# Kernel tuning notes

Measured on AMD Instinct MI355X. Metric: run time of the kernel, lower is better.

The kernel has to match this reference:

```python
import jax, jax.numpy as jnp
import numpy as np

D = 256      # model dim
H = 8        # heads
DK = D // H  # head dim = 32
HID = 4 * D  # mlp hidden = 1024
B, S = 8, 1024
NUM_REL = 10  # rel-pos embedding vocab, padding_idx = 9


def _ln(x, g, b):
    m = jnp.mean(x, axis=-1, keepdims=True)
    v = jnp.var(x, axis=-1, keepdims=True)
    return (x - m) * jax.lax.rsqrt(v + 1e-5) * g + b


def setup_inputs() -> dict:
    key = jax.random.key(0)
    ks = jax.random.split(key, 16)
    s = 0.02
    x = jax.random.normal(ks[0], (B, S, D), jnp.float32)
    rel_pos = jax.random.randint(ks[1], (B, S, S), 0, NUM_REL, jnp.int64)
    adj = jax.random.uniform(ks[2], (B, S, S), jnp.float32)
    # attention params (Linear weights stored as [in, out])
    Wk = jax.random.normal(ks[3], (D, D), jnp.float32) * s
    Wv = jax.random.normal(ks[4], (D, D), jnp.float32) * s
    Wq = jax.random.normal(ks[5], (D, D), jnp.float32) * s
    Wo = jax.random.normal(ks[6], (D, D), jnp.float32) * s
    bk = jnp.zeros((D,)); bv = jnp.zeros((D,)); bq = jnp.zeros((D,)); bo = jnp.zeros((D,))
    # rel-pos embedding tables [10, H], padding row 9 zeroed (padding_idx=9)
    emb_f = (jax.random.normal(ks[7], (NUM_REL, H), jnp.float32) * s).at[NUM_REL - 1].set(0.0)
    emb_b = (jax.random.normal(ks[8], (NUM_REL, H), jnp.float32) * s).at[NUM_REL - 1].set(0.0)
    # GCN-MLP params
    W1 = jax.random.normal(ks[9], (D, HID), jnp.float32) * s
    Wg = jax.random.normal(ks[10], (D, HID), jnp.float32) * s
    W2 = jax.random.normal(ks[11], (HID, D), jnp.float32) * s
    b1 = jnp.zeros((HID,)); bg = jnp.zeros((HID,)); b2 = jnp.zeros((D,))
    return {
        "x": x, "rel_pos": rel_pos, "adj": adj,
        "ln1_g": jnp.ones((D,)), "ln1_b": jnp.zeros((D,)),
        "Wk": Wk, "bk": bk, "Wv": Wv, "bv": bv, "Wq": Wq, "bq": bq,
        "Wo": Wo, "bo": bo, "emb_f": emb_f, "emb_b": emb_b,
        "ln2_g": jnp.ones((D,)), "ln2_b": jnp.zeros((D,)),
        "W1": W1, "b1": b1, "Wg": Wg, "bg": bg, "W2": W2, "b2": b2,
    }


def reference(x, rel_pos, adj, ln1_g, ln1_b, Wk, bk, Wv, bv, Wq, bq, Wo, bo,
              emb_f, emb_b, ln2_g, ln2_b, W1, b1, Wg, bg, W2, b2):
    b_, s_, _ = x.shape
    # --- self-attention block (pre-LN, residual) ---
    xn = _ln(x, ln1_g, ln1_b)
    q = (xn @ Wq + bq).reshape(b_, s_, H, DK).transpose(0, 2, 1, 3)  # [B,H,S,dk]
    k = (xn @ Wk + bk).reshape(b_, s_, H, DK).transpose(0, 2, 1, 3)
    v = (xn @ Wv + bv).reshape(b_, s_, H, DK).transpose(0, 2, 1, 3)
    # multiplicative relative-position bias: [B,S,S,H] -> [B,H,S,S]
    bias = emb_f[rel_pos] + emb_b[jnp.swapaxes(rel_pos, -2, -1)]
    bias = jnp.transpose(bias, (0, 3, 1, 2))
    scores = jnp.einsum('bhqd,bhkd->bhqk', q, k) / np.sqrt(DK).astype(np.float32)
    scores = scores * (1.0 + bias)
    p = jax.nn.softmax(scores, axis=-1)
    o = jnp.einsum('bhqk,bhkd->bhqd', p, v).transpose(0, 2, 1, 3).reshape(b_, s_, D)
    x = x + (o @ Wo + bo)
    # --- GCN feed-forward block (pre-LN, residual) ---
    xn = _ln(x, ln2_g, ln2_b)
    x1 = xn @ W1 + b1                       # [B,S,HID]
    g = xn @ Wg + bg                        # [B,S,HID]
    g1, g2 = jnp.split(g, 2, axis=-1)       # each [B,S,HID/2]
    h = x1 + jnp.concatenate([
        jnp.einsum('bij,bjd->bid', adj, g1),      # adj @ g1
        jnp.einsum('bji,bjd->bid', adj, g2),      # adj.mT @ g2
    ], axis=-1)
    h = jax.nn.relu(h)
    return x + (h @ W2 + b2)
```

## Files before the change

kernel.cpp:

```cpp
#include <hip/hip_runtime.h>
#include <hip/hip_bf16.h>

#define SS 1024
#define DD 256
#define HH 8
#define DKK 32
#define HIDD 1024
#define BB 8

typedef unsigned short ushort_t;
typedef __attribute__((ext_vector_type(8))) short bf16x8;
typedef __attribute__((ext_vector_type(4))) float f32x4;
typedef __attribute__((ext_vector_type(16))) float f32x16;

__device__ __forceinline__ ushort_t f2b(float f) {
    unsigned x = __float_as_uint(f);
    unsigned r = (x + 0x7fffu + ((x >> 16) & 1u)) >> 16;
    return (ushort_t)r;
}
__device__ __forceinline__ float b2f(ushort_t u) {
    return __uint_as_float(((unsigned)u) << 16);
}
__device__ __forceinline__ void gload16(const void* g, void* l) {
    __builtin_amdgcn_global_load_lds(
        (const __attribute__((address_space(1))) unsigned int*)g,
        (__attribute__((address_space(3))) unsigned int*)l, 16, 0, 0);
}

template<bool INBF, bool EMIT>
__global__ __launch_bounds__(256) void ln_kernel(const void* __restrict__ in,
    const float* __restrict__ gamma, const float* __restrict__ beta,
    ushort_t* __restrict__ out, ushort_t* __restrict__ raw)
{
    const int row = blockIdx.x;
    const int t = threadIdx.x;
    float v;
    if (INBF) v = b2f(((const ushort_t*)in)[(long)row * DD + t]);
    else      v = ((const float*)in)[(long)row * DD + t];
    float s = v, s2 = v * v;
#pragma unroll
    for (int off = 1; off < 64; off <<= 1) {
        s += __shfl_xor(s, off);
        s2 += __shfl_xor(s2, off);
    }
    __shared__ float w1[4], w2[4];
    if ((t & 63) == 0) { w1[t >> 6] = s; w2[t >> 6] = s2; }
    __syncthreads();
    s = w1[0] + w1[1] + w1[2] + w1[3];
    s2 = w2[0] + w2[1] + w2[2] + w2[3];
    const float mean = s * (1.f / DD);
    const float var = s2 * (1.f / DD) - mean * mean;
    const float rs = rsqrtf(var + 1e-5f);
    if (EMIT) raw[(long)row * DD + t] = f2b(v);
    out[(long)row * DD + t] = f2b((v - mean) * rs * gamma[t] + beta[t]);
}

__global__ __launch_bounds__(256) void wtrans_all(
    const float* __restrict__ Wq, const float* __restrict__ Wk,
    const float* __restrict__ Wv, const float* __restrict__ Wo,
    const float* __restrict__ W1, const float* __restrict__ Wg,
    const float* __restrict__ W2,
    ushort_t* __restrict__ WqkvT, ushort_t* __restrict__ WoT,
    ushort_t* __restrict__ W1gT, ushort_t* __restrict__ W2T,
    const float* __restrict__ bq, const float* __restrict__ bk,
    const float* __restrict__ bv, const float* __restrict__ b1,
    const float* __restrict__ bg, float* __restrict__ bqkv, float* __restrict__ b1g)
{
    int t = blockIdx.x;
    const int tid = threadIdx.x;
    if (blockIdx.x == 0) {
        for (int i = tid; i < 768; i += 256)
            bqkv[i] = (i < 256) ? bq[i] : ((i < 512) ? bk[i - 256] : bv[i - 512]);
        for (int i = tid; i < 2048; i += 256)
            b1g[i] = (i < 1024) ? b1[i] : bg[i - 1024];
    }
    const float* src; ushort_t* dst; int R, C;
    if (t < 64)        { src = Wq; dst = WqkvT;              R = DD;   C = DD; }
    else if (t < 128)  { src = Wk; dst = WqkvT + 256 * 256;  R = DD;   C = DD;   t -= 64; }
    else if (t < 192)  { src = Wv; dst = WqkvT + 512 * 256;  R = DD;   C = DD;   t -= 128; }
    else if (t < 256)  { src = Wo; dst = WoT;                R = DD;   C = DD;   t -= 192; }
    else if (t < 512)  { src = W1; dst = W1gT;               R = DD;   C = HIDD; t -= 256; }
    else if (t < 768)  { src = Wg; dst = W1gT + 1024 * 256;  R = DD;   C = HIDD; t -= 512; }
    else               { src = W2; dst = W2T;                R = HIDD; C = DD;   t -= 768; }
    const int tilesC = C >> 5;
    const int r0 = (t / tilesC) * 32, c0 = (t % tilesC) * 32;
    __shared__ float tt[32][33];
    const int i = tid >> 3, j0 = (tid & 7) << 2;
    const float4 v = *(const float4*)(src + (long)(r0 + i) * C + c0 + j0);
    tt[i][j0 + 0] = v.x; tt[i][j0 + 1] = v.y; tt[i][j0 + 2] = v.z; tt[i][j0 + 3] = v.w;
    __syncthreads();
    ushort4 o;
    o.x = f2b(tt[j0 + 0][i]); o.y = f2b(tt[j0 + 1][i]);
    o.z = f2b(tt[j0 + 2][i]); o.w = f2b(tt[j0 + 3][i]);
    *(ushort4*)(dst + (long)(c0 + i) * R + r0 + j0) = o;
}

__global__ __launch_bounds__(256) void adjconv(const float* __restrict__ adj,
    ushort_t* __restrict__ adjb, ushort_t* __restrict__ adjTb)
{
    const int c0 = blockIdx.x * 32, r0 = blockIdx.y * 32;
    const long base = (long)blockIdx.z * SS * SS;
    __shared__ float t[32][33];
    const int tid = threadIdx.x;
    const int i = tid >> 3, j0 = (tid & 7) << 2;
    const float4 v = *(const float4*)(adj + base + (long)(r0 + i) * SS + c0 + j0);
    t[i][j0 + 0] = v.x; t[i][j0 + 1] = v.y; t[i][j0 + 2] = v.z; t[i][j0 + 3] = v.w;
    ushort4 oc;
    oc.x = f2b(v.x); oc.y = f2b(v.y); oc.z = f2b(v.z); oc.w = f2b(v.w);
    *(ushort4*)(adjb + base + (long)(r0 + i) * SS + c0 + j0) = oc;
    __syncthreads();
    ushort4 ot;
    ot.x = f2b(t[j0 + 0][i]); ot.y = f2b(t[j0 + 1][i]);
    ot.z = f2b(t[j0 + 2][i]); ot.w = f2b(t[j0 + 3][i]);
    *(ushort4*)(adjTb + base + (long)(c0 + i) * SS + r0 + j0) = ot;
}

__global__ __launch_bounds__(256) void pack_kernel(const int* __restrict__ rp,
    unsigned char* __restrict__ packed)
{
    const int kt = blockIdx.x, qt = blockIdx.y, b = blockIdx.z;
    __shared__ int tA[32][33];
    __shared__ int tB[32][33];
    const int tid = threadIdx.x;
    const int i = tid >> 3;
    const int j0 = (tid & 7) << 2;
    const long base = (long)b * SS * SS;
    const int4 a4 = *(const int4*)(rp + base + (long)(qt * 32 + i) * SS + kt * 32 + j0);
    tA[i][j0 + 0] = a4.x; tA[i][j0 + 1] = a4.y; tA[i][j0 + 2] = a4.z; tA[i][j0 + 3] = a4.w;
    const int4 b4 = *(const int4*)(rp + base + (long)(kt * 32 + i) * SS + qt * 32 + j0);
    tB[i][j0 + 0] = b4.x; tB[i][j0 + 1] = b4.y; tB[i][j0 + 2] = b4.z; tB[i][j0 + 3] = b4.w;
    __syncthreads();
    uchar4 o4;
    o4.x = (unsigned char)(tA[i][j0 + 0] + 10 * tB[j0 + 0][i]);
    o4.y = (unsigned char)(tA[i][j0 + 1] + 10 * tB[j0 + 1][i]);
    o4.z = (unsigned char)(tA[i][j0 + 2] + 10 * tB[j0 + 2][i]);
    o4.w = (unsigned char)(tA[i][j0 + 3] + 10 * tB[j0 + 3][i]);
    *(uchar4*)(packed + base + (long)(qt * 32 + i) * SS + kt * 32 + j0) = o4;
}

template<int MODE, bool RELU, int BN, bool SPLITZ>
__global__ __launch_bounds__(256) void mgemm(
    const ushort_t* __restrict__ A, const ushort_t* __restrict__ BT,
    const float* __restrict__ bias, const void* __restrict__ Res,
    void* __restrict__ C, void* __restrict__ C2,
    int M, int N, int K, int lda, int ldbt, int ldc,
    long sA, long sBT, long sC, long sRes, long tbStride, int tbRows, int nsplit)
{
    int n0, m0, z;
    if (SPLITZ) {
        const int fid = blockIdx.x;
        const int glin = ((fid & 7) << 6) + (fid >> 3);
        z = glin >> 5;
        const int xy = glin & 31;
        n0 = (xy & 3) * BN;
        m0 = (xy >> 2) * 128;
    } else {
        n0 = blockIdx.x * BN; m0 = blockIdx.y * 128; z = blockIdx.z;
    }
    long coff;
    const ushort_t* Ap; const ushort_t* Bp;
    if (SPLITZ) {
        const int zb = z & 7, hf = z >> 3;
        Ap = A + (long)z * sA;
        Bp = BT + (long)zb * sBT + (long)hf * tbStride;
        coff = (long)zb * sC + (long)hf * nsplit;
    } else {
        Ap = A + (long)z * sA;
        Bp = BT + (long)z * sBT;
        coff = (long)z * sC;
    }
    const int tid = threadIdx.x, wid = tid >> 6, lane = tid & 63;
    const int wr = wid >> 1, wc = wid & 1;
    const int l4 = lane & 15, lh = lane >> 4;
    constexpr int NF = BN / 32;
    __shared__ ushort_t Asb[128 * 64];
    __shared__ ushort_t Bsb[BN * 64];
    const int srow = lane >> 3;
    const int scol = 8 * ((lane & 7) ^ srow);
    f32x4 acc[4][NF] = {};
    for (int k0 = 0; k0 < K; k0 += 64) {
#pragma unroll
        for (int i = 0; i < 4; i++) {
            const int l = wid * 4 + i;
            gload16(Ap + (long)(m0 + l * 8 + srow) * lda + k0 + scol, &Asb[l * 512]);
        }
#pragma unroll
        for (int i = 0; i < NF; i++) {
            const int l = wid * NF + i;
            gload16(Bp + (long)(n0 + l * 8 + srow) * ldbt + k0 + scol, &Bsb[l * 512]);
        }
        __syncthreads();
        bf16x8 af[2][4], bfr[2][NF];
#pragma unroll
        for (int mi = 0; mi < 4; mi++) {
            const int row = wr * 64 + mi * 16 + l4;
            const int sw = (row & 7) << 3;
            af[0][mi] = *(const bf16x8*)&Asb[row * 64 + ((lh * 8) ^ sw)];
            af[1][mi] = *(const bf16x8*)&Asb[row * 64 + ((32 + lh * 8) ^ sw)];
        }
#pragma unroll
        for (int nj = 0; nj < NF; nj++) {
            const int row = wc * (BN / 2) + nj * 16 + l4;
            const int sw = (row & 7) << 3;
            bfr[0][nj] = *(const bf16x8*)&Bsb[row * 64 + ((lh * 8) ^ sw)];
            bfr[1][nj] = *(const bf16x8*)&Bsb[row * 64 + ((32 + lh * 8) ^ sw)];
        }
        __builtin_amdgcn_s_setprio(1);
#pragma unroll
        for (int kk = 0; kk < 2; kk++)
#pragma unroll
            for (int mi = 0; mi < 4; mi++)
#pragma unroll
                for (int nj = 0; nj < NF; nj++)
                    acc[mi][nj] = __builtin_amdgcn_mfma_f32_16x16x32_bf16(
                        af[kk][mi], bfr[kk][nj], acc[mi][nj], 0, 0, 0);
        __builtin_amdgcn_s_setprio(0);
        __syncthreads();
    }
#pragma unroll
    for (int mi = 0; mi < 4; mi++) {
#pragma unroll
        for (int nj = 0; nj < NF; nj++) {
            const int n = n0 + wc * (BN / 2) + nj * 16 + l4;
            const int mb = m0 + wr * 64 + mi * 16 + lh * 4;
            const float bv = bias ? bias[n] : 0.f;
            if (MODE == 1) {
                ushort_t* Cp = (ushort_t*)C + coff;
                const ushort_t* Rp = Res ? (const ushort_t*)Res + coff : (const ushort_t*)0;
#pragma unroll
                for (int r = 0; r < 4; r++) {
                    float v = acc[mi][nj][r] + bv;
                    if (Rp) v += b2f(Rp[(long)(mb + r) * ldc + n]);
                    if (RELU) v = fmaxf(v, 0.f);
                    Cp[(long)(mb + r) * ldc + n] = f2b(v);
                }
            } else if (MODE == 4) {
                float* Cp = (float*)C;
                const ushort_t* Rp = (const ushort_t*)Res;
#pragma unroll
                for (int r = 0; r < 4; r++) {
                    float v = acc[mi][nj][r] + bv + b2f(Rp[(long)(mb + r) * ldc + n]);
                    if (RELU) v = fmaxf(v, 0.f);
                    Cp[(long)(mb + r) * ldc + n] = v;
                }
            } else {
                const int nb = n0 + wc * (BN / 2) + nj * 16;
                if (nb < nsplit) {
                    ushort_t* Cp = (ushort_t*)C;
#pragma unroll
                    for (int r = 0; r < 4; r++)
                        Cp[(long)(mb + r) * ldc + n] = f2b(acc[mi][nj][r] + bv);
                } else {
                    ushort_t* Cp = (ushort_t*)C2;
                    const int bidx = mb / tbRows;
                    const int s = mb - bidx * tbRows;
                    ushort4 o4;
                    o4.x = f2b(acc[mi][nj][0] + bv);
                    o4.y = f2b(acc[mi][nj][1] + bv);
                    o4.z = f2b(acc[mi][nj][2] + bv);
                    o4.w = f2b(acc[mi][nj][3] + bv);
                    *(ushort4*)(Cp + (long)bidx * tbStride + (long)(n - nsplit) * tbRows + s) = o4;
                }
            }
        }
    }
}

__global__ __launch_bounds__(256) void attn3(
    const ushort_t* __restrict__ qk, const ushort_t* __restrict__ vt,
    const unsigned char* __restrict__ pkd,
    const float* __restrict__ ef, const float* __restrict__ eb,
    ushort_t* __restrict__ ob)
{
    const int fid = blockIdx.x;
    const int glin = ((fid & 7) << 8) + (fid >> 3);
    const int bh = glin >> 5;
    const int qt = glin & 31;
    const int b = bh >> 3, h = bh & 7;
    const int tid = threadIdx.x;
    const int wid = tid >> 6, lane = tid & 63;
    const int l31 = lane & 31, hi = lane >> 5;
    __shared__ float tm[100];
    __shared__ float cacc[3][64][20];
    __shared__ float cl[3][64];
    if (tid < 100)
        tm[tid] = 0.25506953899092946f
                  * (1.f + ef[(tid % 10) * HH + h] + eb[(tid / 10) * HH + h]);
    __syncthreads();
    const int q0 = qt * 32;
    const ushort_t* qrow = qk + ((long)(b * SS + q0 + l31)) * 512 + h * DKK + hi * 8;
    const bf16x8 qlo = *(const bf16x8*)(qrow);
    const bf16x8 qhi = *(const bf16x8*)(qrow + 16);
    const unsigned char* prow = pkd + ((long)(b * SS + q0 + l31)) * SS;
    const ushort_t* vrow = vt + ((long)(b * DD + h * DKK + l31)) * SS + hi * 8;
    const ushort_t* krow = qk + ((long)(b * SS + l31)) * 512 + 256 + h * DKK + hi * 8;
    f32x16 acc = {};
    float lrun = 0.f;
    const int kbase = wid * 256;
#pragma unroll 2
    for (int it = 0; it < 8; it++) {
        const int kt = kbase + it * 32;
        const ushort_t* kp = krow + (long)kt * 512;
        const bf16x8 klo = *(const bf16x8*)kp;
        const bf16x8 khi = *(const bf16x8*)(kp + 16);
        f32x16 sf = {};
        __builtin_amdgcn_s_setprio(1);
        sf = __builtin_amdgcn_mfma_f32_32x32x16_bf16(klo, qlo, sf, 0, 0, 0);
        sf = __builtin_amdgcn_mfma_f32_32x32x16_bf16(khi, qhi, sf, 0, 0, 0);
        __builtin_amdgcn_s_setprio(0);
        const uint4 u0 = *(const uint4*)(prow + kt);
        const uint4 u1 = *(const uint4*)(prow + kt + 16);
        const unsigned wa = hi ? u0.y : u0.x;
        const unsigned wb = hi ? u0.w : u0.z;
        const unsigned wc2 = hi ? u1.y : u1.x;
        const unsigned wd = hi ? u1.w : u1.z;
        float p[16];
#pragma unroll
        for (int rb = 0; rb < 4; rb++) {
            p[0 + rb]  = __builtin_amdgcn_exp2f(sf[0 + rb]  * tm[(wa  >> (8 * rb)) & 255u]);
            p[4 + rb]  = __builtin_amdgcn_exp2f(sf[4 + rb]  * tm[(wb  >> (8 * rb)) & 255u]);
            p[8 + rb]  = __builtin_amdgcn_exp2f(sf[8 + rb]  * tm[(wc2 >> (8 * rb)) & 255u]);
            p[12 + rb] = __builtin_amdgcn_exp2f(sf[12 + rb] * tm[(wd  >> (8 * rb)) & 255u]);
        }
        float ts = 0.f;
#pragma unroll
        for (int r = 0; r < 16; r++) ts += p[r];
        lrun += ts + __shfl_xor(ts, 32);
        unsigned cw[8];
#pragma unroll
        for (int i = 0; i < 8; i++)
            asm("v_cvt_pk_bf16_f32 %0, %1, %2" : "=v"(cw[i]) : "v"(p[2 * i]), "v"(p[2 * i + 1]));
        unsigned dw[8];
#pragma unroll
        for (int i = 0; i < 8; i++) dw[i] = (unsigned)__shfl_xor((int)cw[i], 32);
        union { unsigned u[8]; bf16x8 v[2]; } fu;
        fu.u[0] = hi ? dw[2] : cw[0]; fu.u[1] = hi ? dw[3] : cw[1];
        fu.u[2] = hi ? cw[2] : dw[0]; fu.u[3] = hi ? cw[3] : dw[1];
        fu.u[4] = hi ? dw[6] : cw[4]; fu.u[5] = hi ? dw[7] : cw[5];
        fu.u[6] = hi ? cw[6] : dw[4]; fu.u[7] = hi ? cw[7] : dw[5];
        const bf16x8 vlo = *(const bf16x8*)(vrow + kt);
        const bf16x8 vhi = *(const bf16x8*)(vrow + kt + 16);
        __builtin_amdgcn_s_setprio(1);
        acc = __builtin_amdgcn_mfma_f32_32x32x16_bf16(vlo, fu.v[0], acc, 0, 0, 0);
        acc = __builtin_amdgcn_mfma_f32_32x32x16_bf16(vhi, fu.v[1], acc, 0, 0, 0);
        __builtin_amdgcn_s_setprio(0);
    }
    if (wid != 0) {
        float* cp = &cacc[wid - 1][lane][0];
#pragma unroll
        for (int r = 0; r < 16; r++) cp[r] = acc[r];
        cl[wid - 1][lane] = lrun;
    }
    __syncthreads();
    if (wid == 0) {
#pragma unroll
        for (int w = 0; w < 3; w++) {
            const float* cp = &cacc[w][lane][0];
#pragma unroll
            for (int r = 0; r < 16; r++) acc[r] += cp[r];
            lrun += cl[w][lane];
        }
        const float invl = 1.f / lrun;
        ushort_t* orow = ob + ((long)(b * SS + q0 + l31)) * DD + h * DKK + 4 * hi;
#pragma unroll
        for (int g = 0; g < 4; g++) {
            ushort4 o4;
            o4.x = f2b(acc[4 * g + 0] * invl);
            o4.y = f2b(acc[4 * g + 1] * invl);
            o4.z = f2b(acc[4 * g + 2] * invl);
            o4.w = f2b(acc[4 * g + 3] * invl);
            *(ushort4*)(orow + 8 * g) = o4;
        }
    }
}

extern "C" void kernel_launch(void* const* d_in, const int* in_sizes, int n_in,
                              void* d_out, int out_size, void* d_ws, size_t ws_size,
                              hipStream_t stream)
{
    const float* x    = (const float*)d_in[0];
    const int*   rp   = (const int*)d_in[1];
    const float* adj  = (const float*)d_in[2];
    const float* ln1g = (const float*)d_in[3];
    const float* ln1b = (const float*)d_in[4];
    const float* Wk   = (const float*)d_in[5];
    const float* bk   = (const float*)d_in[6];
    const float* Wv   = (const float*)d_in[7];
    const float* bv   = (const float*)d_in[8];
    const float* Wq   = (const float*)d_in[9];
    const float* bq   = (const float*)d_in[10];
    const float* Wo   = (const float*)d_in[11];
    const float* bo   = (const float*)d_in[12];
    const float* embf = (const float*)d_in[13];
    const float* embb = (const float*)d_in[14];
    const float* ln2g = (const float*)d_in[15];
    const float* ln2b = (const float*)d_in[16];
    const float* W1   = (const float*)d_in[17];
    const float* b1   = (const float*)d_in[18];
    const float* Wg   = (const float*)d_in[19];
    const float* bg   = (const float*)d_in[20];
    const float* W2   = (const float*)d_in[21];
    const float* b2   = (const float*)d_in[22];
    float* out = (float*)d_out;

    char* ws = (char*)d_ws;
    const long MB = 1ll << 20;
    ushort_t* qkb = (ushort_t*)(ws + 0);
    ushort_t* vtb = (ushort_t*)(ws + 8 * MB);
    ushort_t* obb = (ushort_t*)(ws + 12 * MB);
    unsigned char* pkb = (unsigned char*)(ws + 16 * MB);
    ushort_t* xnb = (ushort_t*)(ws + 24 * MB);
    ushort_t* xb  = (ushort_t*)(ws + 28 * MB);
    ushort_t* x1hb = (ushort_t*)(ws + 0);
    ushort_t* gtb  = (ushort_t*)(ws + 16 * MB);
    ushort_t* x2b  = (ushort_t*)(ws + 32 * MB);
    ushort_t* xn2b = (ushort_t*)(ws + 36 * MB);
    ushort_t* adjb  = (ushort_t*)(ws + 40 * MB);
    ushort_t* adjTb = (ushort_t*)(ws + 56 * MB);
    ushort_t* wT    = (ushort_t*)(ws + 72 * MB);
    ushort_t* WqkvT = wT;
    ushort_t* WoT   = wT + 768 * 256;
    ushort_t* W1gT  = wT + 768 * 256 + 256 * 256;
    ushort_t* W2T   = W1gT + 2048 * 256;
    float* bqkv = (float*)(ws + 75 * MB);
    float* b1g  = bqkv + 768;

    const int rows = BB * SS;
    dim3 blk(256);

    wtrans_all<<<1024, blk, 0, stream>>>(Wq, Wk, Wv, Wo, W1, Wg, W2,
                                         WqkvT, WoT, W1gT, W2T,
                                         bq, bk, bv, b1, bg, bqkv, b1g);
    ln_kernel<false, true><<<rows, blk, 0, stream>>>(x, ln1g, ln1b, xnb, xb);
    mgemm<3, false, 64, false><<<dim3(12, 64, 1), blk, 0, stream>>>(
        xnb, WqkvT, bqkv, nullptr, qkb, vtb, rows, 768, DD, DD, DD, 512,
        0, 0, 0, 0, (long)DD * SS, SS, 512);
    pack_kernel<<<dim3(32, 32, 8), blk, 0, stream>>>(rp, pkb);
    adjconv<<<dim3(32, 32, 8), blk, 0, stream>>>(adj, adjb, adjTb);
    attn3<<<dim3(2048, 1, 1), blk, 0, stream>>>(qkb, vtb, pkb, embf, embb, obb);
    mgemm<1, false, 64, false><<<dim3(4, 64, 1), blk, 0, stream>>>(
        obb, WoT, bo, xb, x2b, nullptr, rows, DD, DD, DD, DD, DD,
        0, 0, 0, 0, 0, 1, 0);
    ln_kernel<true, false><<<rows, blk, 0, stream>>>(x2b, ln2g, ln2b, xn2b, nullptr);
    mgemm<3, false, 128, false><<<dim3(16, 64, 1), blk, 0, stream>>>(
        xn2b, W1gT, b1g, nullptr, x1hb, gtb, rows, 2048, DD, DD, DD, HIDD,
        0, 0, 0, 0, (long)HIDD * SS, SS, 1024);
    mgemm<1, true, 128, true><<<dim3(512, 1, 1), blk, 0, stream>>>(
        adjb, gtb, nullptr, x1hb, x1hb, nullptr, SS, 512, SS, SS, SS, HIDD,
        (long)SS * SS, (long)HIDD * SS, (long)SS * HIDD, 0, (long)512 * SS, SS, 512);
    mgemm<4, false, 64, false><<<dim3(4, 64, 1), blk, 0, stream>>>(
        x1hb, W2T, b2, x2b, out, nullptr, rows, DD, HIDD, HIDD, HIDD, DD,
        0, 0, 0, 0, 0, 1, 0);
}
```

Measured before the change: 337.5 us.

## Store K, V and packed rel-pos in MFMA-fragment tiled layouts for attention

The QKV GEMM epilogue now writes Q row-major, and writes K and V^T into per-(batch,head,32-key) 1KB tiles ordered to match the MFMA operand lanes. The pack kernel likewise stores packed relative-position bytes in 32x32 tiles that match the score fragment layout. The attention loop can then fetch K, V and bias indices with contiguous per-lane 16-byte loads instead of strided row gathers, which aims to improve coalescing and cut memory transactions. In exchange the K stores in the GEMM epilogue become scattered 2-byte writes.

```diff
diff --git a/kernel.cpp b/kernel.cpp
--- a/kernel.cpp
+++ b/kernel.cpp
@@ -135,14 +135,16 @@
     o4.y = (unsigned char)(tA[i][j0 + 1] + 10 * tB[j0 + 1][i]);
     o4.z = (unsigned char)(tA[i][j0 + 2] + 10 * tB[j0 + 2][i]);
     o4.w = (unsigned char)(tA[i][j0 + 3] + 10 * tB[j0 + 3][i]);
-    *(uchar4*)(packed + base + (long)(qt * 32 + i) * SS + kt * 32 + j0) = o4;
+    unsigned char* tile = packed + (((long)b * 32 + qt) * 32 + kt) * 1024;
+    const int jw = j0 >> 3, hi2 = (j0 >> 2) & 1;
+    *(uchar4*)(tile + ((hi2 * 32 + i) * 16) + jw * 4) = o4;
 }
 
 template<int MODE, bool RELU, int BN, bool SPLITZ>
 __global__ __launch_bounds__(256) void mgemm(
     const ushort_t* __restrict__ A, const ushort_t* __restrict__ BT,
     const float* __restrict__ bias, const void* __restrict__ Res,
-    void* __restrict__ C, void* __restrict__ C2,
+    void* __restrict__ C, void* __restrict__ C2, void* __restrict__ C3,
     int M, int N, int K, int lda, int ldbt, int ldc,
     long sA, long sBT, long sC, long sRes, long tbStride, int tbRows, int nsplit)
 {
@@ -242,6 +244,41 @@
                     float v = acc[mi][nj][r] + bv + b2f(Rp[(long)(mb + r) * ldc + n]);
                     if (RELU) v = fmaxf(v, 0.f);
                     Cp[(long)(mb + r) * ldc + n] = v;
+                }
+            } else if (MODE == 5) {
+                const int nb = n0 + wc * (BN / 2) + nj * 16;
+                if (nb < 256) {
+                    ushort_t* Cp = (ushort_t*)C;
+#pragma unroll
+                    for (int r = 0; r < 4; r++)
+                        Cp[(long)(mb + r) * 256 + n] = f2b(acc[mi][nj][r] + bv);
+                } else if (nb < 512) {
+                    ushort_t* Cp = (ushort_t*)C2;
+                    const int h = (n - 256) >> 5, dk = (n - 256) & 31;
+                    const int khalf = dk >> 4, hi2 = (dk >> 3) & 1, e = dk & 7;
+#pragma unroll
+                    for (int r = 0; r < 4; r++) {
+                        const int m = mb + r;
+                        const int bz = m >> 10, s = m & 1023;
+                        const long off = (((long)(bz * 8 + h) * 32 + (s >> 5)) << 10)
+                                       + khalf * 512 + (hi2 * 32 + (s & 31)) * 8 + e;
+                        Cp[off] = f2b(acc[mi][nj][r] + bv);
+                    }
+                } else {
+                    ushort_t* Cp = (ushort_t*)C3;
+                    const int d = n - 512;
+                    const int h = d >> 5, dr = d & 31;
+                    const int bz = mb >> 10, s = mb & 1023;
+                    const int kt32 = s >> 5, kc = s & 31;
+                    const int khalf = kc >> 4, hi2 = (kc >> 3) & 1, e = kc & 7;
+                    const long off = (((long)(bz * 8 + h) * 32 + kt32) << 10)
+                                   + khalf * 512 + (hi2 * 32 + dr) * 8 + e;
+                    ushort4 o4;
+                    o4.x = f2b(acc[mi][nj][0] + bv);
+                    o4.y = f2b(acc[mi][nj][1] + bv);
+                    o4.z = f2b(acc[mi][nj][2] + bv);
+                    o4.w = f2b(acc[mi][nj][3] + bv);
+                    *(ushort4*)(Cp + off) = o4;
                 }
             } else {
                 const int nb = n0 + wc * (BN / 2) + nj * 16;
@@ -267,8 +304,8 @@
 }
 
 __global__ __launch_bounds__(256) void attn3(
-    const ushort_t* __restrict__ qk, const ushort_t* __restrict__ vt,
-    const unsigned char* __restrict__ pkd,
+    const ushort_t* __restrict__ qb, const ushort_t* __restrict__ ktb,
+    const ushort_t* __restrict__ vtb, const unsigned char* __restrict__ pkt,
     const float* __restrict__ ef, const float* __restrict__ eb,
     ushort_t* __restrict__ ob)
 {
@@ -288,39 +325,34 @@
                   * (1.f + ef[(tid % 10) * HH + h] + eb[(tid / 10) * HH + h]);
     __syncthreads();
     const int q0 = qt * 32;
-    const ushort_t* qrow = qk + ((long)(b * SS + q0 + l31)) * 512 + h * DKK + hi * 8;
+    const ushort_t* qrow = qb + ((long)(b * SS + q0 + l31)) * 256 + h * DKK + hi * 8;
     const bf16x8 qlo = *(const bf16x8*)(qrow);
     const bf16x8 qhi = *(const bf16x8*)(qrow + 16);
-    const unsigned char* prow = pkd + ((long)(b * SS + q0 + l31)) * SS;
-    const ushort_t* vrow = vt + ((long)(b * DD + h * DKK + l31)) * SS + hi * 8;
-    const ushort_t* krow = qk + ((long)(b * SS + l31)) * 512 + 256 + h * DKK + hi * 8;
+    const ushort_t* kbase = ktb + (((long)(b * 8 + h) * 32) << 10);
+    const ushort_t* vbase = vtb + (((long)(b * 8 + h) * 32) << 10);
+    const unsigned char* pbase = pkt + (((long)(b * 32 + qt) * 32) << 10);
+    const int lane8 = lane * 8;
     f32x16 acc = {};
     float lrun = 0.f;
-    const int kbase = wid * 256;
 #pragma unroll 2
     for (int it = 0; it < 8; it++) {
-        const int kt = kbase + it * 32;
-        const ushort_t* kp = krow + (long)kt * 512;
-        const bf16x8 klo = *(const bf16x8*)kp;
-        const bf16x8 khi = *(const bf16x8*)(kp + 16);
+        const int kt32 = wid * 8 + it;
+        const ushort_t* ktile = kbase + (kt32 << 10);
+        const bf16x8 klo = *(const bf16x8*)(ktile + lane8);
+        const bf16x8 khi = *(const bf16x8*)(ktile + 512 + lane8);
         f32x16 sf = {};
         __builtin_amdgcn_s_setprio(1);
         sf = __builtin_amdgcn_mfma_f32_32x32x16_bf16(klo, qlo, sf, 0, 0, 0);
         sf = __builtin_amdgcn_mfma_f32_32x32x16_bf16(khi, qhi, sf, 0, 0, 0);
         __builtin_amdgcn_s_setprio(0);
-        const uint4 u0 = *(const uint4*)(prow + kt);
-        const uint4 u1 = *(const uint4*)(prow + kt + 16);
-        const unsigned wa = hi ? u0.y : u0.x;
-        const unsigned wb = hi ? u0.w : u0.z;
-        const unsigned wc2 = hi ? u1.y : u1.x;
-        const unsigned wd = hi ? u1.w : u1.z;
+        const uint4 pw = *(const uint4*)(pbase + (kt32 << 10) + lane * 16);
         float p[16];
 #pragma unroll
         for (int rb = 0; rb < 4; rb++) {
-            p[0 + rb]  = __builtin_amdgcn_exp2f(sf[0 + rb]  * tm[(wa  >> (8 * rb)) & 255u]);
-            p[4 + rb]  = __builtin_amdgcn_exp2f(sf[4 + rb]  * tm[(wb  >> (8 * rb)) & 255u]);
-            p[8 + rb]  = __builtin_amdgcn_exp2f(sf[8 + rb]  * tm[(wc2 >> (8 * rb)) & 255u]);
-            p[12 + rb] = __builtin_amdgcn_exp2f(sf[12 + rb] * tm[(wd  >> (8 * rb)) & 255u]);
+            p[0 + rb]  = __builtin_amdgcn_exp2f(sf[0 + rb]  * tm[(pw.x >> (8 * rb)) & 255u]);
+            p[4 + rb]  = __builtin_amdgcn_exp2f(sf[4 + rb]  * tm[(pw.y >> (8 * rb)) & 255u]);
+            p[8 + rb]  = __builtin_amdgcn_exp2f(sf[8 + rb]  * tm[(pw.z >> (8 * rb)) & 255u]);
+            p[12 + rb] = __builtin_amdgcn_exp2f(sf[12 + rb] * tm[(pw.w >> (8 * rb)) & 255u]);
         }
         float ts = 0.f;
 #pragma unroll
@@ -338,8 +370,9 @@
         fu.u[2] = hi ? cw[2] : dw[0]; fu.u[3] = hi ? cw[3] : dw[1];
         fu.u[4] = hi ? dw[6] : cw[4]; fu.u[5] = hi ? dw[7] : cw[5];
         fu.u[6] = hi ? cw[6] : dw[4]; fu.u[7] = hi ? cw[7] : dw[5];
-        const bf16x8 vlo = *(const bf16x8*)(vrow + kt);
-        const bf16x8 vhi = *(const bf16x8*)(vrow + kt + 16);
+        const ushort_t* vtile = vbase + (kt32 << 10);
+        const bf16x8 vlo = *(const bf16x8*)(vtile + lane8);
+        const bf16x8 vhi = *(const bf16x8*)(vtile + 512 + lane8);
         __builtin_amdgcn_s_setprio(1);
         acc = __builtin_amdgcn_mfma_f32_32x32x16_bf16(vlo, fu.v[0], acc, 0, 0, 0);
         acc = __builtin_amdgcn_mfma_f32_32x32x16_bf16(vhi, fu.v[1], acc, 0, 0, 0);
@@ -405,10 +438,11 @@
 
     char* ws = (char*)d_ws;
     const long MB = 1ll << 20;
-    ushort_t* qkb = (ushort_t*)(ws + 0);
+    ushort_t* qbb = (ushort_t*)(ws + 0);
+    ushort_t* ktb = (ushort_t*)(ws + 4 * MB);
     ushort_t* vtb = (ushort_t*)(ws + 8 * MB);
-    ushort_t* obb = (ushort_t*)(ws + 12 * MB);
-    unsigned char* pkb = (unsigned char*)(ws + 16 * MB);
+    unsigned char* pkt = (unsigned char*)(ws + 12 * MB);
+    ushort_t* obb = (ushort_t*)(ws + 20 * MB);
     ushort_t* xnb = (ushort_t*)(ws + 24 * MB);
     ushort_t* xb  = (ushort_t*)(ws + 28 * MB);
     ushort_t* x1hb = (ushort_t*)(ws + 0);
@@ -432,23 +466,23 @@
                                          WqkvT, WoT, W1gT, W2T,
                                          bq, bk, bv, b1, bg, bqkv, b1g);
     ln_kernel<false, true><<<rows, blk, 0, stream>>>(x, ln1g, ln1b, xnb, xb);
-    mgemm<3, false, 64, false><<<dim3(12, 64, 1), blk, 0, stream>>>(
-        xnb, WqkvT, bqkv, nullptr, qkb, vtb, rows, 768, DD, DD, DD, 512,
-        0, 0, 0, 0, (long)DD * SS, SS, 512);
-    pack_kernel<<<dim3(32, 32, 8), blk, 0, stream>>>(rp, pkb);
+    mgemm<5, false, 64, false><<<dim3(12, 64, 1), blk, 0, stream>>>(
+        xnb, WqkvT, bqkv, nullptr, qbb, ktb, vtb, rows, 768, DD, DD, DD, 256,
+        0, 0, 0, 0, 0, 0, 0);
+    pack_kernel<<<dim3(32, 32, 8), blk, 0, stream>>>(rp, pkt);
     adjconv<<<dim3(32, 32, 8), blk, 0, stream>>>(adj, adjb, adjTb);
-    attn3<<<dim3(2048, 1, 1), blk, 0, stream>>>(qkb, vtb, pkb, embf, embb, obb);
+    attn3<<<dim3(2048, 1, 1), blk, 0, stream>>>(qbb, ktb, vtb, pkt, embf, embb, obb);
     mgemm<1, false, 64, false><<<dim3(4, 64, 1), blk, 0, stream>>>(
-        obb, WoT, bo, xb, x2b, nullptr, rows, DD, DD, DD, DD, DD,
+        obb, WoT, bo, xb, x2b, nullptr, nullptr, rows, DD, DD, DD, DD, DD,
         0, 0, 0, 0, 0, 1, 0);
     ln_kernel<true, false><<<rows, blk, 0, stream>>>(x2b, ln2g, ln2b, xn2b, nullptr);
     mgemm<3, false, 128, false><<<dim3(16, 64, 1), blk, 0, stream>>>(
-        xn2b, W1gT, b1g, nullptr, x1hb, gtb, rows, 2048, DD, DD, DD, HIDD,
+        xn2b, W1gT, b1g, nullptr, x1hb, gtb, nullptr, rows, 2048, DD, DD, DD, HIDD,
         0, 0, 0, 0, (long)HIDD * SS, SS, 1024);
     mgemm<1, true, 128, true><<<dim3(512, 1, 1), blk, 0, stream>>>(
-        adjb, gtb, nullptr, x1hb, x1hb, nullptr, SS, 512, SS, SS, SS, HIDD,
+        adjb, gtb, nullptr, x1hb, x1hb, nullptr, nullptr, SS, 512, SS, SS, SS, HIDD,
         (long)SS * SS, (long)HIDD * SS, (long)SS * HIDD, 0, (long)512 * SS, SS, 512);
     mgemm<4, false, 64, false><<<dim3(4, 64, 1), blk, 0, stream>>>(
-        x1hb, W2T, b2, x2b, out, nullptr, rows, DD, HIDD, HIDD, HIDD, DD,
+        x1hb, W2T, b2, x2b, out, nullptr, nullptr, rows, DD, HIDD, HIDD, HIDD, DD,
         0, 0, 0, 0, 0, 1, 0);
 }
```

New measurement: 309.1 us. 8.4% less time.
